# Optimization experiments

Measured on AMD Instinct MI355X. Metric: run time of the kernel, lower is better.

## Reference

```python
import jax, jax.numpy as jnp
import numpy as np

EPS = 1e-5  # torch BatchNorm1d default eps


def _bn_train(h, gamma, beta):
    # BatchNorm1d in training mode over the edge (batch) axes: biased variance.
    m = jnp.mean(h, axis=(0, 1), keepdims=True)
    v = jnp.mean(jnp.square(h - m), axis=(0, 1), keepdims=True)
    return (h - m) * jax.lax.rsqrt(v + EPS) * gamma + beta


def setup_inputs() -> dict:
    key = jax.random.key(0)
    ks = jax.random.split(key, 12)
    N, F, H = 1024, 128, 128
    s1 = 1.0 / np.sqrt(2 * F)
    s2 = 1.0 / np.sqrt(H)
    return {
        "x": jax.random.normal(ks[0], (N, F), dtype=jnp.float32),
        "W1": jax.random.uniform(ks[1], (H, 2 * F), jnp.float32, -s1, s1),
        "b1": jax.random.uniform(ks[2], (H,), jnp.float32, -s1, s1),
        "W2": jax.random.uniform(ks[3], (H, H), jnp.float32, -s2, s2),
        "b2": jax.random.uniform(ks[4], (H,), jnp.float32, -s2, s2),
        "W3": jax.random.uniform(ks[5], (1, H), jnp.float32, -s2, s2),
        "b3": jax.random.uniform(ks[6], (1,), jnp.float32, -s2, s2),
        "g1": jnp.ones((H,), jnp.float32),
        "be1": jnp.zeros((H,), jnp.float32),
        "g2": jnp.ones((H,), jnp.float32),
        "be2": jnp.zeros((H,), jnp.float32),
    }


def reference(x, W1, b1, W2, b2, W3, b3, g1, be1, g2, be2):
    N, F = x.shape
    # Edge e = i*N + j pairs [x[j], x[i]] (row=j varies fast, col=i slow).
    # First Linear on the concat splits into two low-rank GEMMs + broadcast add,
    # avoiding the [N^2, 2F] materialization (same math as Linear(concat)).
    Wa, Wb = W1[:, :F], W1[:, F:]
    A = x @ Wa.T            # contribution of x[row] = x[j] -> varies over axis 1
    B = x @ Wb.T            # contribution of x[col] = x[i] -> varies over axis 0
    h = A[None, :, :] + B[:, None, :] + b1      # [N, N, H], h[i, j]
    h = jax.nn.relu(_bn_train(h, g1, be1))
    h = jnp.einsum('ijh,kh->ijk', h, W2) + b2   # [N, N, H]
    h = jax.nn.relu(_bn_train(h, g2, be2))
    logits = jnp.einsum('ijh,kh->ijk', h, W3)[..., 0] + b3[0]  # [N, N]
    adj = jax.nn.sigmoid((logits + logits.T) * 0.5)
    adj = adj - jnp.diag(jnp.diag(adj))
    return adj
```

## Files before the change

kernel.cpp:

```cpp
#include <hip/hip_runtime.h>
#include <hip/hip_bf16.h>

typedef __bf16 bf16x8 __attribute__((ext_vector_type(8)));
typedef float  f32x4  __attribute__((ext_vector_type(4)));
typedef float  f32x8  __attribute__((ext_vector_type(8)));

#define EPSV 1e-5f

__global__ __launch_bounds__(256) void k_ab(const float* __restrict__ x,
                                            const float* __restrict__ W1,
                                            const float* __restrict__ W2,
                                            float* __restrict__ A,
                                            float* __restrict__ Bm,
                                            float* __restrict__ gs,
                                            unsigned int* __restrict__ w2p) {
  __shared__ float xs[4 * 128];
  int t = threadIdx.x;
  if (blockIdx.x >= 256) {
    int c = (blockIdx.x - 256) * 256 + t;
    int pair = c & 3;
    int col  = (c >> 2) & 15;
    int quad = (c >> 6) & 3;
    int nt   = (c >> 8) & 7;
    int ks   = (c >> 11) & 3;
    int k = nt * 16 + col;
    int hch = ks * 32 + quad * 8 + pair * 2;
    __bf16 b0 = (__bf16)W2[k * 128 + hch];
    __bf16 b1 = (__bf16)W2[k * 128 + hch + 1];
    unsigned int u0 = *(unsigned short*)&b0, u1 = *(unsigned short*)&b1;
    w2p[c] = u0 | (u1 << 16);
    return;
  }
  int j0 = blockIdx.x * 4;
  for (int idx = t; idx < 512; idx += 256) xs[idx] = x[j0 * 128 + idx];
  __syncthreads();
  int h = t & 127, half = t >> 7;
  const float4* wrow = (const float4*)(W1 + h * 256 + half * 128);
  const float4* xs4 = (const float4*)xs;
  float a0 = 0.f, a1 = 0.f, a2 = 0.f, a3 = 0.f;
#pragma unroll 8
  for (int ch = 0; ch < 32; ++ch) {
    float4 wv = wrow[ch];
    float4 x0 = xs4[ch], x1 = xs4[32 + ch], x2 = xs4[64 + ch], x3 = xs4[96 + ch];
    a0 += wv.x * x0.x + wv.y * x0.y + wv.z * x0.z + wv.w * x0.w;
    a1 += wv.x * x1.x + wv.y * x1.y + wv.z * x1.z + wv.w * x1.w;
    a2 += wv.x * x2.x + wv.y * x2.y + wv.z * x2.z + wv.w * x2.w;
    a3 += wv.x * x3.x + wv.y * x3.y + wv.z * x3.z + wv.w * x3.w;
  }
  float* dst = half ? Bm : A;
  dst[(j0 + 0) * 128 + h] = a0;
  dst[(j0 + 1) * 128 + h] = a1;
  dst[(j0 + 2) * 128 + h] = a2;
  dst[(j0 + 3) * 128 + h] = a3;
  float s = a0 + a1 + a2 + a3;
  float q = a0 * a0 + a1 * a1 + a2 * a2 + a3 * a3;
  atomicAdd(&gs[half * 256 + h], s);
  atomicAdd(&gs[half * 256 + 128 + h], q);
}

__global__ __launch_bounds__(256) void k_fold_apply(const float* __restrict__ gs,
                                                    const float* __restrict__ g1,
                                                    const float* __restrict__ be1,
                                                    const float* __restrict__ A,
                                                    const float* __restrict__ Bm,
                                                    float* __restrict__ Ap,
                                                    float* __restrict__ Bt) {
  __shared__ float sc_s[128], ta_s[128], tb_s[128];
  int t = threadIdx.x;
  if (t < 128) {
    const float inv = 1.f / 1024.f;
    float mA = gs[t] * inv;
    float vA = gs[128 + t] * inv - mA * mA;
    float mB = gs[256 + t] * inv;
    float vB = gs[384 + t] * inv - mB * mB;
    float sc = g1[t] * rsqrtf(vA + vB + EPSV);
    sc_s[t] = sc;
    ta_s[t] = be1[t] - mA * sc;
    tb_s[t] = -mB * sc;
  }
  __syncthreads();
  int idx4 = blockIdx.x * 256 + t;
  int c4 = idx4 & 31;
  float4 sc = ((const float4*)sc_s)[c4];
  float4 ta = ((const float4*)ta_s)[c4];
  float4 tb = ((const float4*)tb_s)[c4];
  float4 a = ((const float4*)A)[idx4];
  float4 b = ((const float4*)Bm)[idx4];
  float4 oa, ob;
  oa.x = fmaf(a.x, sc.x, ta.x); oa.y = fmaf(a.y, sc.y, ta.y);
  oa.z = fmaf(a.z, sc.z, ta.z); oa.w = fmaf(a.w, sc.w, ta.w);
  ob.x = fmaf(b.x, sc.x, tb.x); ob.y = fmaf(b.y, sc.y, tb.y);
  ob.z = fmaf(b.z, sc.z, tb.z); ob.w = fmaf(b.w, sc.w, tb.w);
  int j = idx4 >> 5;
  int h4 = c4 << 2;
  int S = j >> 6, r = (j >> 4) & 3, col = j & 15;
  int ks = h4 >> 5, q = (h4 >> 3) & 3, eh = (h4 >> 2) & 1;
  int dst4 = S * 2048 + eh * 1024 + (r * 4 + ks) * 64 + q * 16 + col;
  ((float4*)Ap)[dst4] = oa;
  ((float4*)Bt)[idx4] = ob;
}

__device__ __forceinline__ bf16x8 build2(f32x4 alo, f32x4 ahi,
                                         const float* __restrict__ bp) {
  f32x4 b0 = *(const f32x4*)bp;
  f32x4 b1 = *(const f32x4*)(bp + 4);
  f32x4 z = {0.f, 0.f, 0.f, 0.f};
  f32x4 h0 = __builtin_elementwise_max(alo + b0, z);
  f32x4 h1 = __builtin_elementwise_max(ahi + b1, z);
  f32x8 h = __builtin_shufflevector(h0, h1, 0, 1, 2, 3, 4, 5, 6, 7);
  return __builtin_convertvector(h, bf16x8);
}

template <int PASS>
__global__ __launch_bounds__(256) void k_pass(
    const float* __restrict__ Ap, const float* __restrict__ Bt,
    const unsigned int* __restrict__ w2p,
    float* __restrict__ sum2, const float* __restrict__ g2,
    const float* __restrict__ be2, const float* __restrict__ W3v,
    const float* __restrict__ b3p, float* __restrict__ L) {
  __shared__ float lds[8192 + 1024];
  float* btl = lds + 8192;
  int t = threadIdx.x;
  int bid = blockIdx.x;
  int bj = bid & 15, bi = bid >> 4;
  int lane = t & 63, w = t >> 6;
  int col = lane & 15, quad = lane >> 4;

  const float* atsrc = Ap + bj * 8192;
#pragma unroll
  for (int it = 0; it < 8; ++it) {
    int g = w * 8 + it;
    __builtin_amdgcn_global_load_lds(
        (const __attribute__((address_space(1))) unsigned int*)(atsrc + g * 256 + lane * 4),
        (__attribute__((address_space(3))) unsigned int*)(lds + g * 256),
        16, 0, 0);
  }
  __builtin_amdgcn_global_load_lds(
      (const __attribute__((address_space(1))) unsigned int*)(Bt + (bi * 8 + w * 2) * 128 + lane * 4),
      (__attribute__((address_space(3))) unsigned int*)(btl + w * 256),
      16, 0, 0);

  bf16x8 bw[4][8];
#pragma unroll
  for (int ks = 0; ks < 4; ++ks)
#pragma unroll
    for (int nt = 0; nt < 8; ++nt)
      bw[ks][nt] = *(const bf16x8*)((const __bf16*)w2p + (((ks * 8 + nt) * 64) + lane) * 8);

  float s1[8], s2[8];
  float al[8], uu[8], w3l[8];
  float b3v = 0.f;
  if (PASS == 1) {
#pragma unroll
    for (int nt = 0; nt < 8; ++nt) { s1[nt] = 0.f; s2[nt] = 0.f; }
  } else {
    b3v = b3p[0];
    const float invM = 1.f / (1024.f * 1024.f);
#pragma unroll
    for (int nt = 0; nt < 8; ++nt) {
      int k = nt * 16 + col;
      float mdot = sum2[k] * invM;
      float var = sum2[128 + k] * invM - mdot * mdot;
      float alv = g2[k] * rsqrtf(var + EPSV);
      al[nt] = alv;
      uu[nt] = be2[k] - mdot * alv;
      w3l[nt] = W3v[k];
    }
  }
  __syncthreads();

  const float* bp0 = btl + w * 256;
  const float* bp1 = bp0 + 128;

  f32x4 pl[4], ph[4];
#pragma unroll
  for (int ks = 0; ks < 4; ++ks) {
    const float* ap = lds + (ks * 64 + lane) * 4;
    pl[ks] = *(const f32x4*)ap;
    ph[ks] = *(const f32x4*)(ap + 4096);
  }

#pragma unroll
  for (int s = 0; s < 4; ++s) {
    f32x4 acc[2][8];
#pragma unroll
    for (int mt = 0; mt < 2; ++mt)
#pragma unroll
      for (int nt = 0; nt < 8; ++nt) acc[mt][nt] = (f32x4){0.f, 0.f, 0.f, 0.f};

    f32x4 cl[4], ch4[4];
#pragma unroll
    for (int ks = 0; ks < 4; ++ks) { cl[ks] = pl[ks]; ch4[ks] = ph[ks]; }
    if (s < 3) {
#pragma unroll
      for (int ks = 0; ks < 4; ++ks) {
        const float* ap = lds + (((s + 1) * 4 + ks) * 64 + lane) * 4;
        pl[ks] = *(const f32x4*)ap;
        ph[ks] = *(const f32x4*)(ap + 4096);
      }
    }

#pragma unroll
    for (int ks = 0; ks < 4; ++ks) {
      bf16x8 a0 = build2(cl[ks], ch4[ks], bp0 + ks * 32 + quad * 8);
      bf16x8 a1 = build2(cl[ks], ch4[ks], bp1 + ks * 32 + quad * 8);
#pragma unroll
      for (int nt = 0; nt < 8; ++nt) {
        acc[0][nt] = __builtin_amdgcn_mfma_f32_16x16x32_bf16(a0, bw[ks][nt], acc[0][nt], 0, 0, 0);
        acc[1][nt] = __builtin_amdgcn_mfma_f32_16x16x32_bf16(a1, bw[ks][nt], acc[1][nt], 0, 0, 0);
      }
    }

    if (PASS == 1) {
#pragma unroll
      for (int nt = 0; nt < 8; ++nt)
#pragma unroll
        for (int mt = 0; mt < 2; ++mt)
#pragma unroll
          for (int r = 0; r < 4; ++r) {
            float d = acc[mt][nt][r];
            s1[nt] += d;
            s2[nt] = fmaf(d, d, s2[nt]);
          }
    } else {
#pragma unroll
      for (int mt = 0; mt < 2; ++mt) {
        float rsum[4] = {0.f, 0.f, 0.f, 0.f};
#pragma unroll
        for (int nt = 0; nt < 8; ++nt)
#pragma unroll
          for (int r = 0; r < 4; ++r) {
            float h = fmaxf(fmaf(acc[mt][nt][r], al[nt], uu[nt]), 0.f);
            rsum[r] = fmaf(h, w3l[nt], rsum[r]);
          }
#pragma unroll
        for (int r = 0; r < 4; ++r) {
          rsum[r] += __shfl_xor(rsum[r], 1);
          rsum[r] += __shfl_xor(rsum[r], 2);
          rsum[r] += __shfl_xor(rsum[r], 4);
          rsum[r] += __shfl_xor(rsum[r], 8);
        }
        if (col == 0) {
          int i = bi * 8 + w * 2 + mt;
#pragma unroll
          for (int r = 0; r < 4; ++r)
            L[i * 1024 + bj * 64 + s * 16 + quad * 4 + r] = rsum[r] + b3v;
        }
      }
    }
  }

  if (PASS == 1) {
#pragma unroll
    for (int nt = 0; nt < 8; ++nt) {
      s1[nt] += __shfl_xor(s1[nt], 16);
      s1[nt] += __shfl_xor(s1[nt], 32);
      s2[nt] += __shfl_xor(s2[nt], 16);
      s2[nt] += __shfl_xor(s2[nt], 32);
    }
    __syncthreads();
    if (lane < 16) {
#pragma unroll
      for (int nt = 0; nt < 8; ++nt) {
        lds[w * 256 + nt * 16 + lane] = s1[nt];
        lds[w * 256 + 128 + nt * 16 + lane] = s2[nt];
      }
    }
    __syncthreads();
    float tot = lds[t] + lds[256 + t] + lds[512 + t] + lds[768 + t];
    atomicAdd(&sum2[t], tot);
  }
}

__global__ __launch_bounds__(256) void k_adj(const float* __restrict__ L,
                                             float* __restrict__ out) {
  int idx = blockIdx.x * 256 + threadIdx.x;
  int i = idx >> 10, j = idx & 1023;
  float a = L[i * 1024 + j];
  float b = L[j * 1024 + i];
  float s = 1.f / (1.f + __expf(-0.5f * (a + b)));
  out[idx] = (i == j) ? 0.f : s;
}

extern "C" void kernel_launch(void* const* d_in, const int* in_sizes, int n_in,
                              void* d_out, int out_size, void* d_ws, size_t ws_size,
                              hipStream_t stream) {
  const float* x   = (const float*)d_in[0];
  const float* W1  = (const float*)d_in[1];
  const float* W2  = (const float*)d_in[3];
  const float* W3  = (const float*)d_in[5];
  const float* b3  = (const float*)d_in[6];
  const float* g1  = (const float*)d_in[7];
  const float* be1 = (const float*)d_in[8];
  const float* g2  = (const float*)d_in[9];
  const float* be2 = (const float*)d_in[10];

  float* ws = (float*)d_ws;
  float* A        = ws;
  float* Bm       = ws + 131072;
  float* Ap       = ws + 262144;
  float* Bt       = ws + 393216;
  unsigned int* w2p = (unsigned int*)(ws + 524288);
  float* gs       = ws + 532480;
  float* sum2     = ws + 532992;
  float* L        = ws + 533248;
  float* out      = (float*)d_out;

  hipMemsetAsync(gs, 0, 768 * sizeof(float), stream);

  k_ab<<<288, 256, 0, stream>>>(x, W1, W2, A, Bm, gs, w2p);
  k_fold_apply<<<128, 256, 0, stream>>>(gs, g1, be1, A, Bm, Ap, Bt);
  k_pass<1><<<2048, 256, 0, stream>>>(Ap, Bt, w2p, sum2, nullptr, nullptr, nullptr, nullptr, nullptr);
  k_pass<2><<<2048, 256, 0, stream>>>(Ap, Bt, w2p, sum2, g2, be2, W3, b3, L);
  k_adj<<<4096, 256, 0, stream>>>(L, out);
}
```

Baseline: 230.1 us.

## Stage W2 fragments in LDS and halve per-block j tile

The W2 B-operand fragments move out of 32 bf16x8 registers per lane and into shared memory via async global-to-LDS loads. They are then read from LDS inside the MFMA loop. The j tile per block drops from 64 to 32 (grid doubles to 4096), with the Ap packing layout changed to match. Bt rows now sit in registers, and the BN2 affine parameters are computed once per block into LDS. The aim is to cut VGPR pressure and raise occupancy, at the cost of more LDS reads per MFMA and more blocks doing redundant W2 loads.

```diff
diff --git a/kernel.cpp b/kernel.cpp
--- a/kernel.cpp
+++ b/kernel.cpp
@@ -93,20 +93,18 @@
   ob.z = fmaf(b.z, sc.z, tb.z); ob.w = fmaf(b.w, sc.w, tb.w);
   int j = idx4 >> 5;
   int h4 = c4 << 2;
-  int S = j >> 6, r = (j >> 4) & 3, col = j & 15;
+  int S = j >> 5, r = (j >> 4) & 1, col = j & 15;
   int ks = h4 >> 5, q = (h4 >> 3) & 3, eh = (h4 >> 2) & 1;
-  int dst4 = S * 2048 + eh * 1024 + (r * 4 + ks) * 64 + q * 16 + col;
+  int dst4 = S * 1024 + eh * 512 + (r * 4 + ks) * 64 + q * 16 + col;
   ((float4*)Ap)[dst4] = oa;
   ((float4*)Bt)[idx4] = ob;
 }
 
-__device__ __forceinline__ bf16x8 build2(f32x4 alo, f32x4 ahi,
-                                         const float* __restrict__ bp) {
-  f32x4 b0 = *(const f32x4*)bp;
-  f32x4 b1 = *(const f32x4*)(bp + 4);
+__device__ __forceinline__ bf16x8 build_r(f32x4 alo, f32x4 ahi,
+                                          f32x4 blo, f32x4 bhi) {
   f32x4 z = {0.f, 0.f, 0.f, 0.f};
-  f32x4 h0 = __builtin_elementwise_max(alo + b0, z);
-  f32x4 h1 = __builtin_elementwise_max(ahi + b1, z);
+  f32x4 h0 = __builtin_elementwise_max(alo + blo, z);
+  f32x4 h1 = __builtin_elementwise_max(ahi + bhi, z);
   f32x8 h = __builtin_shufflevector(h0, h1, 0, 1, 2, 3, 4, 5, 6, 7);
   return __builtin_convertvector(h, bf16x8);
 }
@@ -118,96 +116,82 @@
     float* __restrict__ sum2, const float* __restrict__ g2,
     const float* __restrict__ be2, const float* __restrict__ W3v,
     const float* __restrict__ b3p, float* __restrict__ L) {
-  __shared__ float lds[8192 + 1024];
-  float* btl = lds + 8192;
+  __shared__ float ats[4096];
+  __shared__ __bf16 w2s[16384];
+  __shared__ float red[1024];
   int t = threadIdx.x;
   int bid = blockIdx.x;
-  int bj = bid & 15, bi = bid >> 4;
+  int bj = bid & 31, bi = bid >> 5;
   int lane = t & 63, w = t >> 6;
   int col = lane & 15, quad = lane >> 4;
 
-  const float* atsrc = Ap + bj * 8192;
+  const float* atsrc = Ap + bj * 4096;
+#pragma unroll
+  for (int it = 0; it < 4; ++it) {
+    int base = w * 1024 + it * 256;
+    __builtin_amdgcn_global_load_lds(
+        (const __attribute__((address_space(1))) unsigned int*)(atsrc + base + lane * 4),
+        (__attribute__((address_space(3))) unsigned int*)(ats + base),
+        16, 0, 0);
+  }
 #pragma unroll
   for (int it = 0; it < 8; ++it) {
-    int g = w * 8 + it;
+    int base = w * 512 + it * 64;
     __builtin_amdgcn_global_load_lds(
-        (const __attribute__((address_space(1))) unsigned int*)(atsrc + g * 256 + lane * 4),
-        (__attribute__((address_space(3))) unsigned int*)(lds + g * 256),
+        (const __attribute__((address_space(1))) unsigned int*)(w2p + (base + lane) * 4),
+        (__attribute__((address_space(3))) unsigned int*)((unsigned int*)w2s + base * 4),
         16, 0, 0);
   }
-  __builtin_amdgcn_global_load_lds(
-      (const __attribute__((address_space(1))) unsigned int*)(Bt + (bi * 8 + w * 2) * 128 + lane * 4),
-      (__attribute__((address_space(3))) unsigned int*)(btl + w * 256),
-      16, 0, 0);
-
-  bf16x8 bw[4][8];
-#pragma unroll
-  for (int ks = 0; ks < 4; ++ks)
-#pragma unroll
-    for (int nt = 0; nt < 8; ++nt)
-      bw[ks][nt] = *(const bf16x8*)((const __bf16*)w2p + (((ks * 8 + nt) * 64) + lane) * 8);
+
+  f32x4 btl[2][4], bth[2][4];
+  {
+    const float* br = Bt + (bi * 8 + w * 2) * 128;
+#pragma unroll
+    for (int r = 0; r < 2; ++r)
+#pragma unroll
+      for (int ks = 0; ks < 4; ++ks) {
+        btl[r][ks] = *(const f32x4*)(br + r * 128 + ks * 32 + quad * 8);
+        bth[r][ks] = *(const f32x4*)(br + r * 128 + ks * 32 + quad * 8 + 4);
+      }
+  }
+
+  if (PASS == 2 && t < 128) {
+    const float invM = 1.f / (1024.f * 1024.f);
+    float mdot = sum2[t] * invM;
+    float var = sum2[128 + t] * invM - mdot * mdot;
+    float alv = g2[t] * rsqrtf(var + EPSV);
+    red[t] = alv;
+    red[128 + t] = be2[t] - mdot * alv;
+    red[256 + t] = W3v[t];
+  }
+  __syncthreads();
 
   float s1[8], s2[8];
-  float al[8], uu[8], w3l[8];
-  float b3v = 0.f;
   if (PASS == 1) {
 #pragma unroll
     for (int nt = 0; nt < 8; ++nt) { s1[nt] = 0.f; s2[nt] = 0.f; }
-  } else {
-    b3v = b3p[0];
-    const float invM = 1.f / (1024.f * 1024.f);
-#pragma unroll
-    for (int nt = 0; nt < 8; ++nt) {
-      int k = nt * 16 + col;
-      float mdot = sum2[k] * invM;
-      float var = sum2[128 + k] * invM - mdot * mdot;
-      float alv = g2[k] * rsqrtf(var + EPSV);
-      al[nt] = alv;
-      uu[nt] = be2[k] - mdot * alv;
-      w3l[nt] = W3v[k];
-    }
-  }
-  __syncthreads();
-
-  const float* bp0 = btl + w * 256;
-  const float* bp1 = bp0 + 128;
-
-  f32x4 pl[4], ph[4];
-#pragma unroll
-  for (int ks = 0; ks < 4; ++ks) {
-    const float* ap = lds + (ks * 64 + lane) * 4;
-    pl[ks] = *(const f32x4*)ap;
-    ph[ks] = *(const f32x4*)(ap + 4096);
-  }
-
-#pragma unroll
-  for (int s = 0; s < 4; ++s) {
+  }
+
+#pragma unroll
+  for (int s = 0; s < 2; ++s) {
     f32x4 acc[2][8];
 #pragma unroll
     for (int mt = 0; mt < 2; ++mt)
 #pragma unroll
       for (int nt = 0; nt < 8; ++nt) acc[mt][nt] = (f32x4){0.f, 0.f, 0.f, 0.f};
 
-    f32x4 cl[4], ch4[4];
-#pragma unroll
-    for (int ks = 0; ks < 4; ++ks) { cl[ks] = pl[ks]; ch4[ks] = ph[ks]; }
-    if (s < 3) {
-#pragma unroll
-      for (int ks = 0; ks < 4; ++ks) {
-        const float* ap = lds + (((s + 1) * 4 + ks) * 64 + lane) * 4;
-        pl[ks] = *(const f32x4*)ap;
-        ph[ks] = *(const f32x4*)(ap + 4096);
-      }
-    }
-
 #pragma unroll
     for (int ks = 0; ks < 4; ++ks) {
-      bf16x8 a0 = build2(cl[ks], ch4[ks], bp0 + ks * 32 + quad * 8);
-      bf16x8 a1 = build2(cl[ks], ch4[ks], bp1 + ks * 32 + quad * 8);
+      const float* ap = ats + ((s * 4 + ks) * 64 + lane) * 4;
+      f32x4 alo = *(const f32x4*)ap;
+      f32x4 ahi = *(const f32x4*)(ap + 2048);
+      bf16x8 a0 = build_r(alo, ahi, btl[0][ks], bth[0][ks]);
+      bf16x8 a1 = build_r(alo, ahi, btl[1][ks], bth[1][ks]);
 #pragma unroll
       for (int nt = 0; nt < 8; ++nt) {
-        acc[0][nt] = __builtin_amdgcn_mfma_f32_16x16x32_bf16(a0, bw[ks][nt], acc[0][nt], 0, 0, 0);
-        acc[1][nt] = __builtin_amdgcn_mfma_f32_16x16x32_bf16(a1, bw[ks][nt], acc[1][nt], 0, 0, 0);
+        bf16x8 bv = *(const bf16x8*)(w2s + ((ks * 8 + nt) * 64 + lane) * 8);
+        acc[0][nt] = __builtin_amdgcn_mfma_f32_16x16x32_bf16(a0, bv, acc[0][nt], 0, 0, 0);
+        acc[1][nt] = __builtin_amdgcn_mfma_f32_16x16x32_bf16(a1, bv, acc[1][nt], 0, 0, 0);
       }
     }
 
@@ -223,16 +207,20 @@
             s2[nt] = fmaf(d, d, s2[nt]);
           }
     } else {
+      float b3v = b3p[0];
 #pragma unroll
       for (int mt = 0; mt < 2; ++mt) {
         float rsum[4] = {0.f, 0.f, 0.f, 0.f};
 #pragma unroll
-        for (int nt = 0; nt < 8; ++nt)
+        for (int nt = 0; nt < 8; ++nt) {
+          int k = nt * 16 + col;
+          float alv = red[k], uuv = red[128 + k], w3v = red[256 + k];
 #pragma unroll
           for (int r = 0; r < 4; ++r) {
-            float h = fmaxf(fmaf(acc[mt][nt][r], al[nt], uu[nt]), 0.f);
-            rsum[r] = fmaf(h, w3l[nt], rsum[r]);
+            float h = fmaxf(fmaf(acc[mt][nt][r], alv, uuv), 0.f);
+            rsum[r] = fmaf(h, w3v, rsum[r]);
           }
+        }
 #pragma unroll
         for (int r = 0; r < 4; ++r) {
           rsum[r] += __shfl_xor(rsum[r], 1);
@@ -244,7 +232,7 @@
           int i = bi * 8 + w * 2 + mt;
 #pragma unroll
           for (int r = 0; r < 4; ++r)
-            L[i * 1024 + bj * 64 + s * 16 + quad * 4 + r] = rsum[r] + b3v;
+            L[i * 1024 + bj * 32 + s * 16 + quad * 4 + r] = rsum[r] + b3v;
         }
       }
     }
@@ -258,16 +246,15 @@
       s2[nt] += __shfl_xor(s2[nt], 16);
       s2[nt] += __shfl_xor(s2[nt], 32);
     }
-    __syncthreads();
     if (lane < 16) {
 #pragma unroll
       for (int nt = 0; nt < 8; ++nt) {
-        lds[w * 256 + nt * 16 + lane] = s1[nt];
-        lds[w * 256 + 128 + nt * 16 + lane] = s2[nt];
+        red[w * 256 + nt * 16 + lane] = s1[nt];
+        red[w * 256 + 128 + nt * 16 + lane] = s2[nt];
       }
     }
     __syncthreads();
-    float tot = lds[t] + lds[256 + t] + lds[512 + t] + lds[768 + t];
+    float tot = red[t] + red[256 + t] + red[512 + t] + red[768 + t];
     atomicAdd(&sum2[t], tot);
   }
 }
@@ -310,7 +297,7 @@
 
   k_ab<<<288, 256, 0, stream>>>(x, W1, W2, A, Bm, gs, w2p);
   k_fold_apply<<<128, 256, 0, stream>>>(gs, g1, be1, A, Bm, Ap, Bt);
-  k_pass<1><<<2048, 256, 0, stream>>>(Ap, Bt, w2p, sum2, nullptr, nullptr, nullptr, nullptr, nullptr);
-  k_pass<2><<<2048, 256, 0, stream>>>(Ap, Bt, w2p, sum2, g2, be2, W3, b3, L);
+  k_pass<1><<<4096, 256, 0, stream>>>(Ap, Bt, w2p, sum2, nullptr, nullptr, nullptr, nullptr, nullptr);
+  k_pass<2><<<4096, 256, 0, stream>>>(Ap, Bt, w2p, sum2, g2, be2, W3, b3, L);
   k_adj<<<4096, 256, 0, stream>>>(L, out);
 }
```

Measured after the change: 266.0 us. 15.6% more time.

## Store folded first-layer terms in fp16 and build MFMA operands with packed f16 math

Applied to the files above, without the earlier changes.

The normalized A and B first-layer terms are now written as fp16 in a layout that matches the MFMA operand order. The pass kernels then form ReLU(A+B) with packed half-precision add and max directly on f16x8 vectors, replacing the fp32 build-and-convert-to-bf16 step, and use the f16 MFMA variant. This halves the LDS footprint and global traffic for these operands and removes the per-element conversion cost. B rows are kept in registers instead of LDS, logits are stored as float4, and one barrier is dropped. The trade is that the add and ReLU now run in fp16 instead of fp32, so rounding and range behaviour change.

```diff
diff --git a/kernel.cpp b/kernel.cpp
--- a/kernel.cpp
+++ b/kernel.cpp
@@ -1,9 +1,9 @@
 #include <hip/hip_runtime.h>
 #include <hip/hip_bf16.h>
 
-typedef __bf16 bf16x8 __attribute__((ext_vector_type(8)));
-typedef float  f32x4  __attribute__((ext_vector_type(4)));
-typedef float  f32x8  __attribute__((ext_vector_type(8)));
+typedef _Float16 f16x8 __attribute__((ext_vector_type(8)));
+typedef _Float16 f16x4 __attribute__((ext_vector_type(4)));
+typedef float    f32x4 __attribute__((ext_vector_type(4)));
 
 #define EPSV 1e-5f
 
@@ -25,8 +25,8 @@
     int ks   = (c >> 11) & 3;
     int k = nt * 16 + col;
     int hch = ks * 32 + quad * 8 + pair * 2;
-    __bf16 b0 = (__bf16)W2[k * 128 + hch];
-    __bf16 b1 = (__bf16)W2[k * 128 + hch + 1];
+    _Float16 b0 = (_Float16)W2[k * 128 + hch];
+    _Float16 b1 = (_Float16)W2[k * 128 + hch + 1];
     unsigned int u0 = *(unsigned short*)&b0, u1 = *(unsigned short*)&b1;
     w2p[c] = u0 | (u1 << 16);
     return;
@@ -63,8 +63,8 @@
                                                     const float* __restrict__ be1,
                                                     const float* __restrict__ A,
                                                     const float* __restrict__ Bm,
-                                                    float* __restrict__ Ap,
-                                                    float* __restrict__ Bt) {
+                                                    unsigned int* __restrict__ Apf,
+                                                    unsigned int* __restrict__ Btf) {
   __shared__ float sc_s[128], ta_s[128], tb_s[128];
   int t = threadIdx.x;
   if (t < 128) {
@@ -81,71 +81,65 @@
   __syncthreads();
   int idx4 = blockIdx.x * 256 + t;
   int c4 = idx4 & 31;
-  float4 sc = ((const float4*)sc_s)[c4];
-  float4 ta = ((const float4*)ta_s)[c4];
-  float4 tb = ((const float4*)tb_s)[c4];
-  float4 a = ((const float4*)A)[idx4];
-  float4 b = ((const float4*)Bm)[idx4];
-  float4 oa, ob;
-  oa.x = fmaf(a.x, sc.x, ta.x); oa.y = fmaf(a.y, sc.y, ta.y);
-  oa.z = fmaf(a.z, sc.z, ta.z); oa.w = fmaf(a.w, sc.w, ta.w);
-  ob.x = fmaf(b.x, sc.x, tb.x); ob.y = fmaf(b.y, sc.y, tb.y);
-  ob.z = fmaf(b.z, sc.z, tb.z); ob.w = fmaf(b.w, sc.w, tb.w);
+  f32x4 sc = ((const f32x4*)sc_s)[c4];
+  f32x4 ta = ((const f32x4*)ta_s)[c4];
+  f32x4 tb = ((const f32x4*)tb_s)[c4];
+  f32x4 a = ((const f32x4*)A)[idx4];
+  f32x4 b = ((const f32x4*)Bm)[idx4];
+  f32x4 oa = a * sc + ta;
+  f32x4 ob = b * sc + tb;
+  f16x4 oah = __builtin_convertvector(oa, f16x4);
+  f16x4 obh = __builtin_convertvector(ob, f16x4);
   int j = idx4 >> 5;
   int h4 = c4 << 2;
-  int S = j >> 6, r = (j >> 4) & 3, col = j & 15;
-  int ks = h4 >> 5, q = (h4 >> 3) & 3, eh = (h4 >> 2) & 1;
-  int dst4 = S * 2048 + eh * 1024 + (r * 4 + ks) * 64 + q * 16 + col;
-  ((float4*)Ap)[dst4] = oa;
-  ((float4*)Bt)[idx4] = ob;
-}
-
-__device__ __forceinline__ bf16x8 build2(f32x4 alo, f32x4 ahi,
-                                         const float* __restrict__ bp) {
-  f32x4 b0 = *(const f32x4*)bp;
-  f32x4 b1 = *(const f32x4*)(bp + 4);
-  f32x4 z = {0.f, 0.f, 0.f, 0.f};
-  f32x4 h0 = __builtin_elementwise_max(alo + b0, z);
-  f32x4 h1 = __builtin_elementwise_max(ahi + b1, z);
-  f32x8 h = __builtin_shufflevector(h0, h1, 0, 1, 2, 3, 4, 5, 6, 7);
-  return __builtin_convertvector(h, bf16x8);
+  int S = j >> 6, s = (j >> 4) & 3, col = j & 15;
+  int ks = h4 >> 5, quad = (h4 >> 3) & 3, e0 = h4 & 7;
+  int au = S * 4096 + ((s * 4 + ks) * 64 + quad * 16 + col) * 4 + (e0 >> 1);
+  *(uint2*)(Apf + au) = *(uint2*)&oah;
+  *(uint2*)(Btf + idx4 * 2) = *(uint2*)&obh;
 }
 
 template <int PASS>
 __global__ __launch_bounds__(256) void k_pass(
-    const float* __restrict__ Ap, const float* __restrict__ Bt,
+    const unsigned int* __restrict__ Apf, const unsigned int* __restrict__ Btf,
     const unsigned int* __restrict__ w2p,
     float* __restrict__ sum2, const float* __restrict__ g2,
     const float* __restrict__ be2, const float* __restrict__ W3v,
     const float* __restrict__ b3p, float* __restrict__ L) {
-  __shared__ float lds[8192 + 1024];
-  float* btl = lds + 8192;
+  __shared__ unsigned int ats[4096];
+  __shared__ float red[1024];
   int t = threadIdx.x;
   int bid = blockIdx.x;
   int bj = bid & 15, bi = bid >> 4;
   int lane = t & 63, w = t >> 6;
   int col = lane & 15, quad = lane >> 4;
 
-  const float* atsrc = Ap + bj * 8192;
-#pragma unroll
-  for (int it = 0; it < 8; ++it) {
-    int g = w * 8 + it;
+  const unsigned int* atsrc = Apf + bj * 4096;
+#pragma unroll
+  for (int it = 0; it < 4; ++it) {
+    int g = w * 4 + it;
     __builtin_amdgcn_global_load_lds(
         (const __attribute__((address_space(1))) unsigned int*)(atsrc + g * 256 + lane * 4),
-        (__attribute__((address_space(3))) unsigned int*)(lds + g * 256),
+        (__attribute__((address_space(3))) unsigned int*)(ats + g * 256),
         16, 0, 0);
   }
-  __builtin_amdgcn_global_load_lds(
-      (const __attribute__((address_space(1))) unsigned int*)(Bt + (bi * 8 + w * 2) * 128 + lane * 4),
-      (__attribute__((address_space(3))) unsigned int*)(btl + w * 256),
-      16, 0, 0);
-
-  bf16x8 bw[4][8];
+
+  f16x8 btr[2][4];
+  {
+    int i0 = bi * 8 + w * 2;
+#pragma unroll
+    for (int r = 0; r < 2; ++r)
+#pragma unroll
+      for (int ks = 0; ks < 4; ++ks)
+        btr[r][ks] = *(const f16x8*)((const _Float16*)Btf + (i0 + r) * 128 + ks * 32 + quad * 8);
+  }
+
+  f16x8 bw[4][8];
 #pragma unroll
   for (int ks = 0; ks < 4; ++ks)
 #pragma unroll
     for (int nt = 0; nt < 8; ++nt)
-      bw[ks][nt] = *(const bf16x8*)((const __bf16*)w2p + (((ks * 8 + nt) * 64) + lane) * 8);
+      bw[ks][nt] = *(const f16x8*)((const _Float16*)w2p + (((ks * 8 + nt) * 64) + lane) * 8);
 
   float s1[8], s2[8];
   float al[8], uu[8], w3l[8];
@@ -169,18 +163,9 @@
   }
   __syncthreads();
 
-  const float* bp0 = btl + w * 256;
-  const float* bp1 = bp0 + 128;
-
-  f32x4 pl[4], ph[4];
-#pragma unroll
-  for (int ks = 0; ks < 4; ++ks) {
-    const float* ap = lds + (ks * 64 + lane) * 4;
-    pl[ks] = *(const f32x4*)ap;
-    ph[ks] = *(const f32x4*)(ap + 4096);
-  }
-
-#pragma unroll
+  const f16x8 zz = {(_Float16)0, (_Float16)0, (_Float16)0, (_Float16)0,
+                    (_Float16)0, (_Float16)0, (_Float16)0, (_Float16)0};
+
   for (int s = 0; s < 4; ++s) {
     f32x4 acc[2][8];
 #pragma unroll
@@ -188,26 +173,15 @@
 #pragma unroll
       for (int nt = 0; nt < 8; ++nt) acc[mt][nt] = (f32x4){0.f, 0.f, 0.f, 0.f};
 
-    f32x4 cl[4], ch4[4];
-#pragma unroll
-    for (int ks = 0; ks < 4; ++ks) { cl[ks] = pl[ks]; ch4[ks] = ph[ks]; }
-    if (s < 3) {
-#pragma unroll
-      for (int ks = 0; ks < 4; ++ks) {
-        const float* ap = lds + (((s + 1) * 4 + ks) * 64 + lane) * 4;
-        pl[ks] = *(const f32x4*)ap;
-        ph[ks] = *(const f32x4*)(ap + 4096);
-      }
-    }
-
 #pragma unroll
     for (int ks = 0; ks < 4; ++ks) {
-      bf16x8 a0 = build2(cl[ks], ch4[ks], bp0 + ks * 32 + quad * 8);
-      bf16x8 a1 = build2(cl[ks], ch4[ks], bp1 + ks * 32 + quad * 8);
+      f16x8 af = *(const f16x8*)(ats + ((s * 4 + ks) * 64 + lane) * 4);
+      f16x8 a0 = __builtin_elementwise_max(af + btr[0][ks], zz);
+      f16x8 a1 = __builtin_elementwise_max(af + btr[1][ks], zz);
 #pragma unroll
       for (int nt = 0; nt < 8; ++nt) {
-        acc[0][nt] = __builtin_amdgcn_mfma_f32_16x16x32_bf16(a0, bw[ks][nt], acc[0][nt], 0, 0, 0);
-        acc[1][nt] = __builtin_amdgcn_mfma_f32_16x16x32_bf16(a1, bw[ks][nt], acc[1][nt], 0, 0, 0);
+        acc[0][nt] = __builtin_amdgcn_mfma_f32_16x16x32_f16(a0, bw[ks][nt], acc[0][nt], 0, 0, 0);
+        acc[1][nt] = __builtin_amdgcn_mfma_f32_16x16x32_f16(a1, bw[ks][nt], acc[1][nt], 0, 0, 0);
       }
     }
 
@@ -242,9 +216,9 @@
         }
         if (col == 0) {
           int i = bi * 8 + w * 2 + mt;
-#pragma unroll
-          for (int r = 0; r < 4; ++r)
-            L[i * 1024 + bj * 64 + s * 16 + quad * 4 + r] = rsum[r] + b3v;
+          float4 v = make_float4(rsum[0] + b3v, rsum[1] + b3v,
+                                 rsum[2] + b3v, rsum[3] + b3v);
+          *(float4*)(&L[i * 1024 + bj * 64 + s * 16 + quad * 4]) = v;
         }
       }
     }
@@ -258,16 +232,15 @@
       s2[nt] += __shfl_xor(s2[nt], 16);
       s2[nt] += __shfl_xor(s2[nt], 32);
     }
+    if (lane < 16) {
+#pragma unroll
+      for (int nt = 0; nt < 8; ++nt) {
+        red[w * 256 + nt * 16 + lane] = s1[nt];
+        red[w * 256 + 128 + nt * 16 + lane] = s2[nt];
+      }
+    }
     __syncthreads();
-    if (lane < 16) {
-#pragma unroll
-      for (int nt = 0; nt < 8; ++nt) {
-        lds[w * 256 + nt * 16 + lane] = s1[nt];
-        lds[w * 256 + 128 + nt * 16 + lane] = s2[nt];
-      }
-    }
-    __syncthreads();
-    float tot = lds[t] + lds[256 + t] + lds[512 + t] + lds[768 + t];
+    float tot = red[t] + red[256 + t] + red[512 + t] + red[768 + t];
     atomicAdd(&sum2[t], tot);
   }
 }
@@ -296,21 +269,21 @@
   const float* be2 = (const float*)d_in[10];
 
   float* ws = (float*)d_ws;
-  float* A        = ws;
-  float* Bm       = ws + 131072;
-  float* Ap       = ws + 262144;
-  float* Bt       = ws + 393216;
-  unsigned int* w2p = (unsigned int*)(ws + 524288);
-  float* gs       = ws + 532480;
-  float* sum2     = ws + 532992;
-  float* L        = ws + 533248;
-  float* out      = (float*)d_out;
+  float* A          = ws;
+  float* Bm         = ws + 131072;
+  unsigned int* Apf = (unsigned int*)(ws + 262144);
+  unsigned int* Btf = (unsigned int*)(ws + 327680);
+  unsigned int* w2p = (unsigned int*)(ws + 393216);
+  float* gs         = ws + 401408;
+  float* sum2       = ws + 401920;
+  float* L          = ws + 402176;
+  float* out        = (float*)d_out;
 
   hipMemsetAsync(gs, 0, 768 * sizeof(float), stream);
 
   k_ab<<<288, 256, 0, stream>>>(x, W1, W2, A, Bm, gs, w2p);
-  k_fold_apply<<<128, 256, 0, stream>>>(gs, g1, be1, A, Bm, Ap, Bt);
-  k_pass<1><<<2048, 256, 0, stream>>>(Ap, Bt, w2p, sum2, nullptr, nullptr, nullptr, nullptr, nullptr);
-  k_pass<2><<<2048, 256, 0, stream>>>(Ap, Bt, w2p, sum2, g2, be2, W3, b3, L);
+  k_fold_apply<<<128, 256, 0, stream>>>(gs, g1, be1, A, Bm, Apf, Btf);
+  k_pass<1><<<2048, 256, 0, stream>>>(Apf, Btf, w2p, sum2, nullptr, nullptr, nullptr, nullptr, nullptr);
+  k_pass<2><<<2048, 256, 0, stream>>>(Apf, Btf, w2p, sum2, g2, be2, W3, b3, L);
   k_adj<<<4096, 256, 0, stream>>>(L, out);
 }
```

New measurement: 217.4 us. -5.5%, faster.
